# Kernel optimization log

Measured on AMD Instinct MI355X. Metric: run time of the kernel, lower is better.

Reference implementation:

```python
import jax, jax.numpy as jnp
import numpy as np

N_HEAD = 16
NEG_BIG = 1e10


def setup_inputs() -> dict:
    key = jax.random.key(0)
    ks = jax.random.split(key, 4)
    B, T, D = 2, 2048, 1024
    x = jax.random.normal(ks[0], (B, T, D), dtype=jnp.float32)
    w_attn = jax.random.normal(ks[1], (D, 3 * D), dtype=jnp.float32) * 0.02
    b_attn = jnp.zeros((3 * D,), dtype=jnp.float32)
    w_proj = jax.random.normal(ks[2], (D, D), dtype=jnp.float32) * 0.02
    b_proj = jnp.zeros((D,), dtype=jnp.float32)
    return {"x": x, "w_attn": w_attn, "b_attn": b_attn, "w_proj": w_proj, "b_proj": b_proj}


def reference(x, w_attn, b_attn, w_proj, b_proj):
    B, T, D = x.shape
    H = N_HEAD
    dh = D // H
    # fused QKV projection (Conv1d == addmm: x @ W + b)
    qkv = x @ w_attn + b_attn                      # [B, T, 3D]
    q, k, v = jnp.split(qkv, 3, axis=-1)
    # split heads -> [B, H, T, dh]
    q = q.reshape(B, T, H, dh).transpose(0, 2, 1, 3)
    k = k.reshape(B, T, H, dh).transpose(0, 2, 1, 3)
    v = v.reshape(B, T, H, dh).transpose(0, 2, 1, 3)
    # scores; repo scales by 1/sqrt(n_head) (its idiosyncrasy, kept faithfully)
    w = jnp.einsum('bhqd,bhkd->bhqk', q, k) / jnp.sqrt(jnp.float32(H))
    # causal mask via repo formula: w*b - 1e10*(1-b), b = tril ones
    b = jnp.tril(jnp.ones((T, T), dtype=w.dtype))
    w = w * b - NEG_BIG * (1.0 - b)
    w = jax.nn.softmax(w, axis=-1)
    a = jnp.einsum('bhqk,bhkd->bhqd', w, v)        # [B, H, T, dh]
    # merge heads
    a = a.transpose(0, 2, 1, 3).reshape(B, T, D)
    a = a @ w_proj + b_proj
    present = jnp.stack([k, v])                     # [2, B, H, T, dh]
    return a, present
```

## Files before the change

### kernel.cpp

```cpp
#include <hip/hip_runtime.h>
#include <hip/hip_bf16.h>

typedef __hip_bfloat16 bf16;
typedef unsigned short ush;
typedef __attribute__((ext_vector_type(8))) short bf16x8;
typedef __attribute__((ext_vector_type(4))) float f32x4;

#define BB 2
#define TT 2048
#define DD 1024
#define HH 16
#define DHH 64
#define MM (BB*TT)
#define N3 (3*DD)

__device__ __forceinline__ bf16  f2b(float x){ return __float2bfloat16(x); }
__device__ __forceinline__ ush   f2bu(float x){ bf16 h = __float2bfloat16(x); return *(ush*)&h; }

#define GLOAD_LDS(gp, lp) \
    __builtin_amdgcn_global_load_lds( \
        (const __attribute__((address_space(1))) void*)(gp), \
        (__attribute__((address_space(3))) void*)(lp), 16, 0, 0)

__global__ __launch_bounds__(256) void cvt_x(
    const float* __restrict__ src, ush* __restrict__ dst)
{
    const size_t i = ((size_t)blockIdx.x * 256 + threadIdx.x) * 8;
    float4 a = *(const float4*)&src[i];
    float4 b = *(const float4*)&src[i + 4];
    ushort4 u0; u0.x = f2bu(a.x); u0.y = f2bu(a.y); u0.z = f2bu(a.z); u0.w = f2bu(a.w);
    ushort4 u1; u1.x = f2bu(b.x); u1.y = f2bu(b.y); u1.z = f2bu(b.z); u1.w = f2bu(b.w);
    *(ushort4*)&dst[i] = u0;
    *(ushort4*)&dst[i + 4] = u1;
}

__global__ __launch_bounds__(256) void transpose_cvt(
    const float* __restrict__ src, ush* __restrict__ dst, int R, int C)
{
    __shared__ ush T[64][68];
    const int tid = threadIdx.x;
    const int c0 = blockIdx.x * 64;
    const int r0 = blockIdx.y * 64;

    #pragma unroll
    for (int it = 0; it < 4; it++) {
        int idx = it * 256 + tid;
        int i = idx >> 4, jf = idx & 15;
        float4 v = *(const float4*)&src[(size_t)(r0 + i) * C + c0 + jf * 4];
        T[jf * 4 + 0][i] = f2bu(v.x);
        T[jf * 4 + 1][i] = f2bu(v.y);
        T[jf * 4 + 2][i] = f2bu(v.z);
        T[jf * 4 + 3][i] = f2bu(v.w);
    }
    __syncthreads();
    #pragma unroll
    for (int it = 0; it < 4; it++) {
        int idx = it * 256 + tid;
        int j = idx >> 4, i4 = idx & 15;
        *(ushort4*)&dst[(size_t)(c0 + j) * R + r0 + i4 * 4] =
            *(const ushort4*)&T[j][i4 * 4];
    }
}

__global__ __launch_bounds__(256) void qkv_mfma(
    const ush* __restrict__ xbf, const ush* __restrict__ wT,
    const float* __restrict__ bias,
    bf16* __restrict__ qws, float* __restrict__ kout, float* __restrict__ vout,
    ush* __restrict__ kbf, ush* __restrict__ vtb, int write_bf)
{
    __shared__ __align__(16) ush As[128 * 32];
    __shared__ __align__(16) ush Bs[128 * 32];

    const int tid  = threadIdx.x;
    const int lane = tid & 63;
    const int w    = tid >> 6;
    const int n16  = lane & 15;
    const int quad = lane >> 4;
    const int row0 = blockIdx.y * 128;
    const int col0 = blockIdx.x * 128;
    const int wrow = (w >> 1) * 64;
    const int wcol = (w & 1) * 64;

    f32x4 acc[4][4];
    #pragma unroll
    for (int mb = 0; mb < 4; mb++)
        #pragma unroll
        for (int nb = 0; nb < 4; nb++) acc[mb][nb] = (f32x4){0.f,0.f,0.f,0.f};

    for (int kk0 = 0; kk0 < DD; kk0 += 32) {
        __syncthreads();
        #pragma unroll
        for (int it = 0; it < 2; it++) {
            int c = it * 256 + tid;
            int r = c >> 2, co = (c & 3) * 8;
            GLOAD_LDS(&xbf[(size_t)(row0 + r) * DD + kk0 + co], &As[c * 8]);
            GLOAD_LDS(&wT[(size_t)(col0 + r) * DD + kk0 + co], &Bs[c * 8]);
        }
        __syncthreads();

        bf16x8 af[4];
        #pragma unroll
        for (int mb = 0; mb < 4; mb++)
            af[mb] = *(const bf16x8*)&As[(wrow + mb * 16 + n16) * 32 + quad * 8];
        #pragma unroll
        for (int nb = 0; nb < 4; nb++) {
            bf16x8 bfr = *(const bf16x8*)&Bs[(wcol + nb * 16 + n16) * 32 + quad * 8];
            #pragma unroll
            for (int mb = 0; mb < 4; mb++)
                acc[mb][nb] = __builtin_amdgcn_mfma_f32_16x16x32_bf16(
                    af[mb], bfr, acc[mb][nb], 0, 0, 0);
        }
    }

    const float qsc = write_bf ? 0.36067376022224085f : 1.0f;

    #pragma unroll
    for (int nb = 0; nb < 4; nb++) {
        const int gc = col0 + wcol + nb * 16 + n16;
        const float bv = bias[gc];
        const int which = gc >> 10;
        const int h = (gc & 1023) >> 6;
        const int d = gc & 63;
        #pragma unroll
        for (int mb = 0; mb < 4; mb++) {
            float vv[4];
            #pragma unroll
            for (int reg = 0; reg < 4; reg++) vv[reg] = acc[mb][nb][reg] + bv;
            const int gr0 = row0 + wrow + mb * 16 + quad * 4;
            const int b_ = gr0 >> 11, t0 = gr0 & 2047;
            const int bh = b_ * HH + h;
            const size_t tbase = ((size_t)bh * TT + t0) * DHH + d;
            if (which == 0) {
                #pragma unroll
                for (int reg = 0; reg < 4; reg++)
                    qws[tbase + (size_t)reg * DHH] = f2b(vv[reg] * qsc);
            } else if (which == 1) {
                #pragma unroll
                for (int reg = 0; reg < 4; reg++) kout[tbase + (size_t)reg * DHH] = vv[reg];
                if (write_bf) {
                    #pragma unroll
                    for (int reg = 0; reg < 4; reg++)
                        kbf[tbase + (size_t)reg * DHH] = f2bu(vv[reg]);
                }
            } else {
                #pragma unroll
                for (int reg = 0; reg < 4; reg++) vout[tbase + (size_t)reg * DHH] = vv[reg];
                if (write_bf) {
                    ushort4 u;
                    u.x = f2bu(vv[0]); u.y = f2bu(vv[1]);
                    u.z = f2bu(vv[2]); u.w = f2bu(vv[3]);
                    *(ushort4*)&vtb[((size_t)bh * DHH + d) * TT + t0] = u;
                }
            }
        }
    }
}

__global__ __launch_bounds__(256) void flash_attn_v5(
    const ush* __restrict__ qin, const ush* __restrict__ kbf,
    const ush* __restrict__ vtb, bf16* __restrict__ attn)
{
    __shared__ __align__(16) ush Ks[64][72];
    __shared__ __align__(16) ush Vt[64][72];
    __shared__ __align__(16) ush Ps[4][16][72];

    const int tid  = threadIdx.x;
    const int lane = tid & 63;
    const int w    = tid >> 6;
    const int n16  = lane & 15;
    const int quad = lane >> 4;
    const int bh = blockIdx.y;
    const int qi = (bh & 8) ? (31 - (int)blockIdx.x) : (int)blockIdx.x;
    const int q0 = qi * 64;
    const ush* Qb  = qin + (size_t)bh * TT * DHH;
    const ush* Kb  = kbf + (size_t)bh * TT * DHH;
    const ush* Vtb = vtb + (size_t)bh * DHH * TT;
    const int b_ = bh >> 4, h = bh & 15;

    const ush* Qp = Qb + (size_t)(q0 + w * 16 + n16) * DHH + quad * 8;
    const bf16x8 qa0 = *(const bf16x8*)&Qp[0];
    const bf16x8 qa1 = *(const bf16x8*)&Qp[32];

    const int r0c = tid >> 3, c8c = (tid & 7) * 8;
    const int r1c = (256 + tid) >> 3, c8c1 = ((256 + tid) & 7) * 8;

    bf16x8 kst[2], vst[2];
    {
        const ush* Kp = Kb;
        const ush* Vp = Vtb;
        kst[0] = *(const bf16x8*)&Kp[(size_t)r0c * DHH + c8c];
        kst[1] = *(const bf16x8*)&Kp[(size_t)r1c * DHH + c8c1];
        vst[0] = *(const bf16x8*)&Vp[(size_t)r0c * TT + c8c];
        vst[1] = *(const bf16x8*)&Vp[(size_t)r1c * TT + c8c1];
    }

    f32x4 o[4];
    #pragma unroll
    for (int db = 0; db < 4; db++) o[db] = (f32x4){0.f, 0.f, 0.f, 0.f};
    float lsum[4] = {0.f, 0.f, 0.f, 0.f};

    const int rloc = w * 16 + quad * 4;

    for (int kt = 0; kt <= qi; kt++) {
        __syncthreads();
        *(bf16x8*)&Ks[r0c][c8c]  = kst[0];
        *(bf16x8*)&Ks[r1c][c8c1] = kst[1];
        *(bf16x8*)&Vt[r0c][c8c]  = vst[0];
        *(bf16x8*)&Vt[r1c][c8c1] = vst[1];
        __syncthreads();

        if (kt < qi) {
            const ush* Kp = Kb + (size_t)((kt + 1) * 64) * DHH;
            const ush* Vp = Vtb + (kt + 1) * 64;
            kst[0] = *(const bf16x8*)&Kp[(size_t)r0c * DHH + c8c];
            kst[1] = *(const bf16x8*)&Kp[(size_t)r1c * DHH + c8c1];
            vst[0] = *(const bf16x8*)&Vp[(size_t)r0c * TT + c8c];
            vst[1] = *(const bf16x8*)&Vp[(size_t)r1c * TT + c8c1];
        }

        f32x4 s[4];
        #pragma unroll
        for (int cb = 0; cb < 4; cb++) {
            bf16x8 kb0 = *(const bf16x8*)&Ks[cb * 16 + n16][quad * 8];
            bf16x8 kb1 = *(const bf16x8*)&Ks[cb * 16 + n16][32 + quad * 8];
            f32x4 acc = (f32x4){0.f, 0.f, 0.f, 0.f};
            acc = __builtin_amdgcn_mfma_f32_16x16x32_bf16(qa0, kb0, acc, 0, 0, 0);
            acc = __builtin_amdgcn_mfma_f32_16x16x32_bf16(qa1, kb1, acc, 0, 0, 0);
            s[cb] = acc;
        }

        if (kt == qi) {
            #pragma unroll
            for (int reg = 0; reg < 4; reg++) {
                #pragma unroll
                for (int cb = 0; cb < 4; cb++) {
                    float p = exp2f(s[cb][reg]);
                    if (cb * 16 + n16 > rloc + reg) p = 0.f;
                    lsum[reg] += p;
                    Ps[w][quad * 4 + reg][cb * 16 + n16] = f2bu(p);
                }
            }
        } else {
            #pragma unroll
            for (int reg = 0; reg < 4; reg++) {
                #pragma unroll
                for (int cb = 0; cb < 4; cb++) {
                    float p = exp2f(s[cb][reg]);
                    lsum[reg] += p;
                    Ps[w][quad * 4 + reg][cb * 16 + n16] = f2bu(p);
                }
            }
        }

        bf16x8 pa0 = *(const bf16x8*)&Ps[w][n16][quad * 8];
        bf16x8 pa1 = *(const bf16x8*)&Ps[w][n16][32 + quad * 8];
        #pragma unroll
        for (int db = 0; db < 4; db++) {
            bf16x8 vb0 = *(const bf16x8*)&Vt[db * 16 + n16][quad * 8];
            bf16x8 vb1 = *(const bf16x8*)&Vt[db * 16 + n16][32 + quad * 8];
            o[db] = __builtin_amdgcn_mfma_f32_16x16x32_bf16(pa0, vb0, o[db], 0, 0, 0);
            o[db] = __builtin_amdgcn_mfma_f32_16x16x32_bf16(pa1, vb1, o[db], 0, 0, 0);
        }
    }

    const int grow_base = q0 + rloc;
    #pragma unroll
    for (int reg = 0; reg < 4; reg++) {
        float ls = lsum[reg];
        #pragma unroll
        for (int off = 1; off < 16; off <<= 1)
            ls += __shfl_xor(ls, off);
        const float il = 1.0f / ls;
        const int t_ = grow_base + reg;
        bf16* outr = attn + ((size_t)(b_ * TT + t_)) * DD + h * 64 + n16;
        #pragma unroll
        for (int db = 0; db < 4; db++)
            outr[db * 16] = f2b(o[db][reg] * il);
    }
}

__global__ __launch_bounds__(256) void flash_attn_mfma(
    const bf16* __restrict__ qin, const float* __restrict__ kin,
    const float* __restrict__ vin, bf16* __restrict__ attn)
{
    __shared__ __align__(16) ush Qs[64][72];
    __shared__ __align__(16) ush Ks[64][72];
    __shared__ __align__(16) ush Vt[64][72];
    __shared__ __align__(16) ush Ps[4][16][72];

    const int tid  = threadIdx.x;
    const int lane = tid & 63;
    const int w    = tid >> 6;
    const int n16  = lane & 15;
    const int quad = lane >> 4;
    const int qi = blockIdx.x;
    const int bh = blockIdx.y;
    const int q0 = qi * 64;

    const ush*   Qp = (const ush*)qin + ((size_t)bh * TT + q0) * DHH;
    const float* Kb = kin + (size_t)bh * TT * DHH;
    const float* Vb = vin + (size_t)bh * TT * DHH;

    #pragma unroll
    for (int it = 0; it < 4; it++) {
        int idx = (it * 256 + tid) * 4;
        int r = idx >> 6, d = idx & 63;
        *(ushort4*)&Qs[r][d] = *(const ushort4*)&Qp[idx];
    }

    f32x4 o[4];
    #pragma unroll
    for (int db = 0; db < 4; db++) o[db] = (f32x4){0.f, 0.f, 0.f, 0.f};
    float m_old[4] = {-1e30f, -1e30f, -1e30f, -1e30f};
    float l_run[4] = {0.f, 0.f, 0.f, 0.f};

    for (int kt = 0; kt <= qi; kt++) {
        const float* Kp = Kb + (size_t)(kt * 64) * DHH;
        const float* Vp = Vb + (size_t)(kt * 64) * DHH;
        __syncthreads();
        #pragma unroll
        for (int it = 0; it < 4; it++) {
            int idx = (it * 256 + tid) * 4;
            int c = idx >> 6, d = idx & 63;
            float4 kv = *(const float4*)&Kp[idx];
            ushort4 kb;
            kb.x = f2bu(kv.x); kb.y = f2bu(kv.y); kb.z = f2bu(kv.z); kb.w = f2bu(kv.w);
            *(ushort4*)&Ks[c][d] = kb;
        }
        #pragma unroll
        for (int it = 0; it < 4; it++) {
            int c = tid & 63, d0 = (tid >> 6) * 4 + it * 16;
            float4 vv = *(const float4*)&Vp[c * 64 + d0];
            Vt[d0 + 0][c] = f2bu(vv.x);
            Vt[d0 + 1][c] = f2bu(vv.y);
            Vt[d0 + 2][c] = f2bu(vv.z);
            Vt[d0 + 3][c] = f2bu(vv.w);
        }
        __syncthreads();

        bf16x8 qa0 = *(const bf16x8*)&Qs[w * 16 + n16][quad * 8];
        bf16x8 qa1 = *(const bf16x8*)&Qs[w * 16 + n16][32 + quad * 8];
        f32x4 s[4];
        #pragma unroll
        for (int cb = 0; cb < 4; cb++) {
            bf16x8 kb0 = *(const bf16x8*)&Ks[cb * 16 + n16][quad * 8];
            bf16x8 kb1 = *(const bf16x8*)&Ks[cb * 16 + n16][32 + quad * 8];
            f32x4 acc = (f32x4){0.f, 0.f, 0.f, 0.f};
            acc = __builtin_amdgcn_mfma_f32_16x16x32_bf16(qa0, kb0, acc, 0, 0, 0);
            acc = __builtin_amdgcn_mfma_f32_16x16x32_bf16(qa1, kb1, acc, 0, 0, 0);
            s[cb] = acc;
        }

        const int grow_base = q0 + w * 16 + quad * 4;
        const int gcol_base = kt * 64 + n16;
        #pragma unroll
        for (int reg = 0; reg < 4; reg++) {
            float sv[4];
            float pm = -1e30f;
            #pragma unroll
            for (int cb = 0; cb < 4; cb++) {
                float v = s[cb][reg] * 0.25f;
                if (gcol_base + cb * 16 > grow_base + reg) v = -1e10f;
                sv[cb] = v;
                pm = fmaxf(pm, v);
            }
            #pragma unroll
            for (int off = 1; off < 16; off <<= 1)
                pm = fmaxf(pm, __shfl_xor(pm, off));
            float mnew = fmaxf(m_old[reg], pm);
            float alpha = __expf(m_old[reg] - mnew);
            float ps = 0.f;
            #pragma unroll
            for (int cb = 0; cb < 4; cb++) {
                float p = __expf(sv[cb] - mnew);
                Ps[w][quad * 4 + reg][cb * 16 + n16] = f2bu(p);
                ps += p;
            }
            #pragma unroll
            for (int off = 1; off < 16; off <<= 1)
                ps += __shfl_xor(ps, off);
            l_run[reg] = l_run[reg] * alpha + ps;
            m_old[reg] = mnew;
            #pragma unroll
            for (int db = 0; db < 4; db++) o[db][reg] *= alpha;
        }
        __syncthreads();

        bf16x8 pa0 = *(const bf16x8*)&Ps[w][n16][quad * 8];
        bf16x8 pa1 = *(const bf16x8*)&Ps[w][n16][32 + quad * 8];
        #pragma unroll
        for (int db = 0; db < 4; db++) {
            bf16x8 vb0 = *(const bf16x8*)&Vt[db * 16 + n16][quad * 8];
            bf16x8 vb1 = *(const bf16x8*)&Vt[db * 16 + n16][32 + quad * 8];
            o[db] = __builtin_amdgcn_mfma_f32_16x16x32_bf16(pa0, vb0, o[db], 0, 0, 0);
            o[db] = __builtin_amdgcn_mfma_f32_16x16x32_bf16(pa1, vb1, o[db], 0, 0, 0);
        }
    }

    const int b_ = bh >> 4, h = bh & 15;
    #pragma unroll
    for (int reg = 0; reg < 4; reg++) {
        const float il = 1.0f / l_run[reg];
        const int t_ = q0 + w * 16 + quad * 4 + reg;
        bf16* outr = attn + ((size_t)(b_ * TT + t_)) * DD + h * 64 + n16;
        #pragma unroll
        for (int db = 0; db < 4; db++)
            outr[db * 16] = f2b(o[db][reg] * il);
    }
}

__global__ __launch_bounds__(256) void proj_mfma(
    const ush* __restrict__ a, const ush* __restrict__ wpT,
    const float* __restrict__ bias, float* __restrict__ out)
{
    __shared__ __align__(16) ush As[128 * 32];
    __shared__ __align__(16) ush Bs[128 * 32];

    const int tid  = threadIdx.x;
    const int lane = tid & 63;
    const int w    = tid >> 6;
    const int n16  = lane & 15;
    const int quad = lane >> 4;
    const int row0 = blockIdx.y * 128;
    const int col0 = blockIdx.x * 128;
    const int wrow = (w >> 1) * 64;
    const int wcol = (w & 1) * 64;

    f32x4 acc[4][4];
    #pragma unroll
    for (int mb = 0; mb < 4; mb++)
        #pragma unroll
        for (int nb = 0; nb < 4; nb++) acc[mb][nb] = (f32x4){0.f,0.f,0.f,0.f};

    for (int kk0 = 0; kk0 < DD; kk0 += 32) {
        __syncthreads();
        #pragma unroll
        for (int it = 0; it < 2; it++) {
            int c = it * 256 + tid;
            int r = c >> 2, co = (c & 3) * 8;
            GLOAD_LDS(&a[(size_t)(row0 + r) * DD + kk0 + co], &As[c * 8]);
            GLOAD_LDS(&wpT[(size_t)(col0 + r) * DD + kk0 + co], &Bs[c * 8]);
        }
        __syncthreads();

        bf16x8 af[4];
        #pragma unroll
        for (int mb = 0; mb < 4; mb++)
            af[mb] = *(const bf16x8*)&As[(wrow + mb * 16 + n16) * 32 + quad * 8];
        #pragma unroll
        for (int nb = 0; nb < 4; nb++) {
            bf16x8 bfr = *(const bf16x8*)&Bs[(wcol + nb * 16 + n16) * 32 + quad * 8];
            #pragma unroll
            for (int mb = 0; mb < 4; mb++)
                acc[mb][nb] = __builtin_amdgcn_mfma_f32_16x16x32_bf16(
                    af[mb], bfr, acc[mb][nb], 0, 0, 0);
        }
    }

    #pragma unroll
    for (int nb = 0; nb < 4; nb++) {
        const int gc = col0 + wcol + nb * 16 + n16;
        const float bv = bias[gc];
        #pragma unroll
        for (int mb = 0; mb < 4; mb++) {
            #pragma unroll
            for (int reg = 0; reg < 4; reg++) {
                const int gr = row0 + wrow + mb * 16 + quad * 4 + reg;
                out[(size_t)gr * DD + gc] = acc[mb][nb][reg] + bv;
            }
        }
    }
}

extern "C" void kernel_launch(void* const* d_in, const int* in_sizes, int n_in,
                              void* d_out, int out_size, void* d_ws, size_t ws_size,
                              hipStream_t stream) {
    const float *x = nullptr, *w_attn = nullptr, *b_attn = nullptr,
                *w_proj = nullptr, *b_proj = nullptr;
    for (int i = 0; i < n_in; i++) {
        switch (in_sizes[i]) {
            case 4194304: x      = (const float*)d_in[i]; break;
            case 3145728: w_attn = (const float*)d_in[i]; break;
            case 3072:    b_attn = (const float*)d_in[i]; break;
            case 1048576: w_proj = (const float*)d_in[i]; break;
            case 1024:    b_proj = (const float*)d_in[i]; break;
            default: break;
        }
    }
    if (!x || !w_attn || !b_attn || !w_proj || !b_proj) return;

    float* out_a = (float*)d_out;
    float* out_k = out_a + (size_t)MM * DD;
    float* out_v = out_k + (size_t)BB * HH * TT * DHH;

    const size_t MB = 1024 * 1024;
    char* wsc = (char*)d_ws;
    ush*  wT     = (ush*)(wsc + 0);
    bf16* attnws = (bf16*)(wsc + 0);
    bf16* qws    = (bf16*)(wsc + 8 * MB);
    ush*  wpT    = (ush*)(wsc + 8 * MB);
    ush*  xbf    = (ush*)d_out;

    if (ws_size >= 32 * MB) {
        ush* kbf = (ush*)(wsc + 16 * MB);
        ush* vtb = (ush*)(wsc + 24 * MB);
        cvt_x<<<dim3(MM * DD / (256 * 8)), 256, 0, stream>>>(x, xbf);
        transpose_cvt<<<dim3(N3 / 64, DD / 64), 256, 0, stream>>>(w_attn, wT, DD, N3);
        qkv_mfma<<<dim3(N3 / 128, MM / 128), 256, 0, stream>>>(
            xbf, wT, b_attn, qws, out_k, out_v, kbf, vtb, 1);
        flash_attn_v5<<<dim3(TT / 64, BB * HH), 256, 0, stream>>>(
            (const ush*)qws, kbf, vtb, attnws);
        transpose_cvt<<<dim3(DD / 64, DD / 64), 256, 0, stream>>>(w_proj, wpT, DD, DD);
        proj_mfma<<<dim3(DD / 128, MM / 128), 256, 0, stream>>>(
            (const ush*)attnws, wpT, b_proj, out_a);
    } else if (ws_size >= 16 * MB) {
        cvt_x<<<dim3(MM * DD / (256 * 8)), 256, 0, stream>>>(x, xbf);
        transpose_cvt<<<dim3(N3 / 64, DD / 64), 256, 0, stream>>>(w_attn, wT, DD, N3);
        qkv_mfma<<<dim3(N3 / 128, MM / 128), 256, 0, stream>>>(
            xbf, wT, b_attn, qws, out_k, out_v, nullptr, nullptr, 0);
        flash_attn_mfma<<<dim3(TT / 64, BB * HH), 256, 0, stream>>>(
            qws, out_k, out_v, attnws);
        transpose_cvt<<<dim3(DD / 64, DD / 64), 256, 0, stream>>>(w_proj, wpT, DD, DD);
        proj_mfma<<<dim3(DD / 128, MM / 128), 256, 0, stream>>>(
            (const ush*)attnws, wpT, b_proj, out_a);
    }
}
```

Measured before the change: 200.5 us.

## Keep attention probabilities in registers via transposed QK^T and fuse prep kernels

The attention kernel now computes S^T by swapping the MFMA operands and permuting the K row indices, so each lane's exp'd scores already sit in the A-operand layout for the PV MFMA. This removes the shared-memory round trip for P (the Ps buffer and its writes and reads) and simplifies the row-sum reduction to two shuffles. Separately, the x conversion and the w_attn transpose-convert are merged into one launch to save a kernel launch. The risk is in the index permutation and causal mask mapping, which must match the MFMA lane layout exactly.

```diff
diff --git a/kernel.cpp b/kernel.cpp
--- a/kernel.cpp
+++ b/kernel.cpp
@@ -22,16 +22,45 @@
         (const __attribute__((address_space(1))) void*)(gp), \
         (__attribute__((address_space(3))) void*)(lp), 16, 0, 0)
 
-__global__ __launch_bounds__(256) void cvt_x(
-    const float* __restrict__ src, ush* __restrict__ dst)
+__global__ __launch_bounds__(256) void prep_fused(
+    const float* __restrict__ x, const float* __restrict__ w_attn,
+    ush* __restrict__ xbf, ush* __restrict__ wT)
 {
-    const size_t i = ((size_t)blockIdx.x * 256 + threadIdx.x) * 8;
-    float4 a = *(const float4*)&src[i];
-    float4 b = *(const float4*)&src[i + 4];
-    ushort4 u0; u0.x = f2bu(a.x); u0.y = f2bu(a.y); u0.z = f2bu(a.z); u0.w = f2bu(a.w);
-    ushort4 u1; u1.x = f2bu(b.x); u1.y = f2bu(b.y); u1.z = f2bu(b.z); u1.w = f2bu(b.w);
-    *(ushort4*)&dst[i] = u0;
-    *(ushort4*)&dst[i + 4] = u1;
+    __shared__ ush T[64][68];
+    const int tid = threadIdx.x;
+    const int bid = blockIdx.x;
+
+    if (bid < 2048) {
+        const size_t i = ((size_t)bid * 256 + tid) * 8;
+        float4 a = *(const float4*)&x[i];
+        float4 b = *(const float4*)&x[i + 4];
+        ushort4 u0; u0.x = f2bu(a.x); u0.y = f2bu(a.y); u0.z = f2bu(a.z); u0.w = f2bu(a.w);
+        ushort4 u1; u1.x = f2bu(b.x); u1.y = f2bu(b.y); u1.z = f2bu(b.z); u1.w = f2bu(b.w);
+        *(ushort4*)&xbf[i] = u0;
+        *(ushort4*)&xbf[i + 4] = u1;
+        return;
+    }
+    const int j  = bid - 2048;
+    const int c0 = (j % 48) * 64;
+    const int r0 = (j / 48) * 64;
+    #pragma unroll
+    for (int it = 0; it < 4; it++) {
+        int idx = it * 256 + tid;
+        int i = idx >> 4, jf = idx & 15;
+        float4 v = *(const float4*)&w_attn[(size_t)(r0 + i) * N3 + c0 + jf * 4];
+        T[jf * 4 + 0][i] = f2bu(v.x);
+        T[jf * 4 + 1][i] = f2bu(v.y);
+        T[jf * 4 + 2][i] = f2bu(v.z);
+        T[jf * 4 + 3][i] = f2bu(v.w);
+    }
+    __syncthreads();
+    #pragma unroll
+    for (int it = 0; it < 4; it++) {
+        int idx = it * 256 + tid;
+        int jj = idx >> 4, i4 = idx & 15;
+        *(ushort4*)&wT[(size_t)(c0 + jj) * DD + r0 + i4 * 4] =
+            *(const ushort4*)&T[jj][i4 * 4];
+    }
 }
 
 __global__ __launch_bounds__(256) void transpose_cvt(
@@ -156,13 +185,12 @@
     }
 }
 
-__global__ __launch_bounds__(256) void flash_attn_v5(
+__global__ __launch_bounds__(256) void flash_attn_v6(
     const ush* __restrict__ qin, const ush* __restrict__ kbf,
     const ush* __restrict__ vtb, bf16* __restrict__ attn)
 {
     __shared__ __align__(16) ush Ks[64][72];
     __shared__ __align__(16) ush Vt[64][72];
-    __shared__ __align__(16) ush Ps[4][16][72];
 
     const int tid  = threadIdx.x;
     const int lane = tid & 63;
@@ -184,6 +212,9 @@
     const int r0c = tid >> 3, c8c = (tid & 7) * 8;
     const int r1c = (256 + tid) >> 3, c8c1 = ((256 + tid) & 7) * 8;
 
+    const int rsb = ((n16 >> 2) << 3) + ((n16 & 1) << 2) + ((n16 & 2) << 4);
+    const int rq  = w * 16 + n16;
+
     bf16x8 kst[2], vst[2];
     {
         const ush* Kp = Kb;
@@ -197,9 +228,7 @@
     f32x4 o[4];
     #pragma unroll
     for (int db = 0; db < 4; db++) o[db] = (f32x4){0.f, 0.f, 0.f, 0.f};
-    float lsum[4] = {0.f, 0.f, 0.f, 0.f};
-
-    const int rloc = w * 16 + quad * 4;
+    float lsum = 0.f;
 
     for (int kt = 0; kt <= qi; kt++) {
         __syncthreads();
@@ -220,40 +249,49 @@
 
         f32x4 s[4];
         #pragma unroll
-        for (int cb = 0; cb < 4; cb++) {
-            bf16x8 kb0 = *(const bf16x8*)&Ks[cb * 16 + n16][quad * 8];
-            bf16x8 kb1 = *(const bf16x8*)&Ks[cb * 16 + n16][32 + quad * 8];
-            f32x4 acc = (f32x4){0.f, 0.f, 0.f, 0.f};
-            acc = __builtin_amdgcn_mfma_f32_16x16x32_bf16(qa0, kb0, acc, 0, 0, 0);
-            acc = __builtin_amdgcn_mfma_f32_16x16x32_bf16(qa1, kb1, acc, 0, 0, 0);
-            s[cb] = acc;
-        }
-
+        for (int m = 0; m < 4; m++) {
+            bf16x8 kb0 = *(const bf16x8*)&Ks[rsb + m][quad * 8];
+            bf16x8 kb1 = *(const bf16x8*)&Ks[rsb + m][32 + quad * 8];
+            f32x4 a4 = (f32x4){0.f, 0.f, 0.f, 0.f};
+            a4 = __builtin_amdgcn_mfma_f32_16x16x32_bf16(kb0, qa0, a4, 0, 0, 0);
+            a4 = __builtin_amdgcn_mfma_f32_16x16x32_bf16(kb1, qa1, a4, 0, 0, 0);
+            s[m] = a4;
+        }
+
+        float p[4][4];
         if (kt == qi) {
             #pragma unroll
-            for (int reg = 0; reg < 4; reg++) {
+            for (int m = 0; m < 4; m++) {
                 #pragma unroll
-                for (int cb = 0; cb < 4; cb++) {
-                    float p = exp2f(s[cb][reg]);
-                    if (cb * 16 + n16 > rloc + reg) p = 0.f;
-                    lsum[reg] += p;
-                    Ps[w][quad * 4 + reg][cb * 16 + n16] = f2bu(p);
+                for (int reg = 0; reg < 4; reg++) {
+                    const int kl = quad * 8 + m + ((reg & 1) << 2) + ((reg >> 1) << 5);
+                    float pv = exp2f(s[m][reg]);
+                    if (kl > rq) pv = 0.f;
+                    p[m][reg] = pv;
+                    lsum += pv;
                 }
             }
         } else {
             #pragma unroll
-            for (int reg = 0; reg < 4; reg++) {
+            for (int m = 0; m < 4; m++) {
                 #pragma unroll
-                for (int cb = 0; cb < 4; cb++) {
-                    float p = exp2f(s[cb][reg]);
-                    lsum[reg] += p;
-                    Ps[w][quad * 4 + reg][cb * 16 + n16] = f2bu(p);
+                for (int reg = 0; reg < 4; reg++) {
+                    float pv = exp2f(s[m][reg]);
+                    p[m][reg] = pv;
+                    lsum += pv;
                 }
             }
         }
 
-        bf16x8 pa0 = *(const bf16x8*)&Ps[w][n16][quad * 8];
-        bf16x8 pa1 = *(const bf16x8*)&Ps[w][n16][32 + quad * 8];
+        bf16x8 pa0, pa1;
+        #pragma unroll
+        for (int m = 0; m < 4; m++) {
+            pa0[m]     = (short)f2bu(p[m][0]);
+            pa0[m + 4] = (short)f2bu(p[m][1]);
+            pa1[m]     = (short)f2bu(p[m][2]);
+            pa1[m + 4] = (short)f2bu(p[m][3]);
+        }
+
         #pragma unroll
         for (int db = 0; db < 4; db++) {
             bf16x8 vb0 = *(const bf16x8*)&Vt[db * 16 + n16][quad * 8];
@@ -263,15 +301,13 @@
         }
     }
 
-    const int grow_base = q0 + rloc;
+    float ls = lsum;
+    ls += __shfl_xor(ls, 16);
+    ls += __shfl_xor(ls, 32);
     #pragma unroll
     for (int reg = 0; reg < 4; reg++) {
-        float ls = lsum[reg];
-        #pragma unroll
-        for (int off = 1; off < 16; off <<= 1)
-            ls += __shfl_xor(ls, off);
-        const float il = 1.0f / ls;
-        const int t_ = grow_base + reg;
+        const float il = 1.0f / __shfl(ls, quad * 4 + reg);
+        const int t_ = q0 + w * 16 + quad * 4 + reg;
         bf16* outr = attn + ((size_t)(b_ * TT + t_)) * DD + h * 64 + n16;
         #pragma unroll
         for (int db = 0; db < 4; db++)
@@ -504,18 +540,16 @@
     if (ws_size >= 32 * MB) {
         ush* kbf = (ush*)(wsc + 16 * MB);
         ush* vtb = (ush*)(wsc + 24 * MB);
-        cvt_x<<<dim3(MM * DD / (256 * 8)), 256, 0, stream>>>(x, xbf);
-        transpose_cvt<<<dim3(N3 / 64, DD / 64), 256, 0, stream>>>(w_attn, wT, DD, N3);
+        prep_fused<<<dim3(2048 + 768), 256, 0, stream>>>(x, w_attn, xbf, wT);
         qkv_mfma<<<dim3(N3 / 128, MM / 128), 256, 0, stream>>>(
             xbf, wT, b_attn, qws, out_k, out_v, kbf, vtb, 1);
-        flash_attn_v5<<<dim3(TT / 64, BB * HH), 256, 0, stream>>>(
+        flash_attn_v6<<<dim3(TT / 64, BB * HH), 256, 0, stream>>>(
             (const ush*)qws, kbf, vtb, attnws);
         transpose_cvt<<<dim3(DD / 64, DD / 64), 256, 0, stream>>>(w_proj, wpT, DD, DD);
         proj_mfma<<<dim3(DD / 128, MM / 128), 256, 0, stream>>>(
             (const ush*)attnws, wpT, b_proj, out_a);
     } else if (ws_size >= 16 * MB) {
-        cvt_x<<<dim3(MM * DD / (256 * 8)), 256, 0, stream>>>(x, xbf);
-        transpose_cvt<<<dim3(N3 / 64, DD / 64), 256, 0, stream>>>(w_attn, wT, DD, N3);
+        prep_fused<<<dim3(2048 + 768), 256, 0, stream>>>(x, w_attn, xbf, wT);
         qkv_mfma<<<dim3(N3 / 128, MM / 128), 256, 0, stream>>>(
             xbf, wT, b_attn, qws, out_k, out_v, nullptr, nullptr, 0);
         flash_attn_mfma<<<dim3(TT / 64, BB * HH), 256, 0, stream>>>(
```

New measurement: 190.9 us. 1.05x faster.
